# Optimization experiments

Measured on AMD Instinct MI355X. Metric: run time of the kernel, lower is better.

## Reference

```python
import jax, jax.numpy as jnp
import numpy as np

B, T, C, J = 2048, 128, 3, 25   # batch, frames, coords, joints
E = 64                          # structure elements (n_elements)


def setup_inputs() -> dict:
    key = jax.random.key(0)
    k1, k2 = jax.random.split(key)
    x = jax.random.normal(k1, (B, T, C, J), dtype=jnp.float32)
    centres = jax.random.uniform(k2, (E, 2), dtype=jnp.float32)
    sharpness = jnp.full((E, 2), 3.0, dtype=jnp.float32)  # torch init: ones*3
    return {"x": x, "centres": centres, "sharpness": sharpness}


def _mst_deaths(Dm):
    """Prim's MST over dense distance matrix Dm [n,n].
    The multiset of MST edge weights equals the finite death times of the
    0-dim Vietoris-Rips persistence diagram (births are all 0)."""
    n = Dm.shape[0]
    in_tree0 = jnp.zeros(n, dtype=bool).at[0].set(True)

    def step(carry, _):
        mind, in_tree = carry
        masked = jnp.where(in_tree, jnp.inf, mind)  # distance from tree to each node
        j = jnp.argmin(masked)
        w = masked[j]                               # weight of edge added to MST
        in_tree = in_tree.at[j].set(True)
        mind = jnp.minimum(mind, Dm[j])
        return (mind, in_tree), w

    (_, _), deaths = jax.lax.scan(step, (Dm[0], in_tree0), None, length=n - 1)
    return deaths  # [n-1]


def reference(x, centres, sharpness):
    # --- dense preprocessing ---
    h = x.mean(1)                           # [B, C, J]
    h = h[..., :, None] - h[..., None, :]   # [B, C, J, J] pairwise coord diffs
    h = h.mean(-3)                          # [B, J, J]
    h = jnp.sqrt((h * h).sum(axis=1))       # torch.norm(., 2, dim=1) -> [B, J]
    lo, hi = h.min(), h.max()
    rng = hi - lo
    safe = rng > 1e-8
    h = jnp.where(safe, (h - lo) / jnp.where(safe, rng, 1.0), jnp.zeros_like(h))

    # --- Vietoris-Rips dim-0 persistence on point cloud h: B points in J dims ---
    sq = (h * h).sum(-1)
    d2 = sq[:, None] + sq[None, :] - 2.0 * (h @ h.T)       # [B, B]
    Dm = jnp.sqrt(jnp.maximum(d2, 1e-12))
    deaths = _mst_deaths(Dm)                               # [B-1]
    pd = jnp.stack([jnp.zeros_like(deaths), deaths], -1)[None]  # [1, P, 2]

    # --- StructureElementLayer: out[b,e] = sum_p exp(-sum_d s[e,d]^2 (pd-c)^2) ---
    s2 = sharpness * sharpness                             # [E, 2]
    diff = pd[:, :, None, :] - centres[None, None, :, :]   # [1, P, E, 2]
    out = jnp.exp(-(diff * diff * s2).sum(-1)).sum(1)      # [1, E]
    return out
```

## Files before the change

### kernel.cpp

```cpp
#include <hip/hip_runtime.h>
#include <math.h>

#define B_N 2048
#define T_N 128
#define C_N 3
#define J_N 25
#define E_N 64
#define TC  (T_N*C_N)
#define TCJ (TC*J_N)
#define NQ4 (TCJ/4)
#define NC  128

#define D_OFF      0
#define H_OFF      (B_N*B_N)
#define BLO_OFF    (H_OFF + B_N*J_N)
#define BHI_OFF    (BLO_OFF + B_N)
#define DEATHS_OFF (BHI_OFF + B_N)
#define BEST_OFF   (DEATHS_OFF + B_N)
#define COMP_OFF   (BEST_OFF + 4*B_N)
#define GC_OFF     (COMP_OFF + 2*B_N)
#define DC_OFF     (GC_OFF + 2)

typedef unsigned long long u64;
#define U64MAX 0xFFFFFFFFFFFFFFFFull
#define U32INF 0xFFFFFFFFu

__global__ void __launch_bounds__(256) k_reduce(const float* __restrict__ x,
                                                float* __restrict__ ws) {
    __shared__ float4 part[250];
    __shared__ float S[100];
    __shared__ float Mj[25];
    const int t = threadIdx.x, b = blockIdx.x;
    const float4* x4 = (const float4*)(x + (size_t)b * TCJ);
    if (t < 250) {
        float4 a; a.x = a.y = a.z = a.w = 0.f;
        for (int idx = t; idx < NQ4; idx += 250) {
            float4 v = x4[idx];
            a.x += v.x; a.y += v.y; a.z += v.z; a.w += v.w;
        }
        part[t] = a;
    }
    __syncthreads();
    if (t < 25) {
        float4 s = part[t];
        #pragma unroll
        for (int g = 1; g < 10; ++g) {
            float4 v = part[t + 25 * g];
            s.x += v.x; s.y += v.y; s.z += v.z; s.w += v.w;
        }
        S[4*t] = s.x; S[4*t+1] = s.y; S[4*t+2] = s.z; S[4*t+3] = s.w;
    }
    __syncthreads();
    if (t < 25) Mj[t] = (S[t] + S[t+25] + S[t+50] + S[t+75]) * (1.0f / 384.0f);
    __syncthreads();
    if (t < 25) {
        float mj = Mj[t], acc = 0.f;
        #pragma unroll
        for (int i = 0; i < J_N; ++i) { float d = Mj[i] - mj; acc += d * d; }
        float hv = sqrtf(acc);
        ws[H_OFF + b * J_N + t] = hv;
        S[t] = hv;
    }
    __syncthreads();
    if (t == 0) {
        float lo = S[0], hi = S[0];
        #pragma unroll
        for (int i = 1; i < J_N; ++i) { lo = fminf(lo, S[i]); hi = fmaxf(hi, S[i]); }
        ws[BLO_OFF + b] = lo;
        ws[BHI_OFF + b] = hi;
    }
}

__global__ void __launch_bounds__(256) k_dist(float* ws) {
    __shared__ float A[32][27], Bsh[32][27];
    const int t = threadIdx.x;
    const int rowA = blockIdx.x * 32, rowB = blockIdx.y * 32;
    const float* h = ws + H_OFF;
    for (int idx = t; idx < 32 * J_N; idx += 256) {
        int r = idx / J_N, c = idx % J_N;
        A[r][c]   = h[(rowA + r) * J_N + c];
        Bsh[r][c] = h[(rowB + r) * J_N + c];
    }
    __syncthreads();
    const int tx = t & 31, ty = t >> 5;
    float* D = ws + D_OFF;
    #pragma unroll
    for (int rr = 0; rr < 4; ++rr) {
        const int r = ty + rr * 8;
        float acc = 0.f;
        #pragma unroll
        for (int k = 0; k < J_N; ++k) {
            float d = A[r][k] - Bsh[tx][k];
            acc += d * d;
        }
        D[(size_t)(rowA + r) * B_N + rowB + tx] = sqrtf(fmaxf(acc, 1e-12f));
    }
}

__global__ void __launch_bounds__(1024) k_scan0(float* __restrict__ ws) {
    const int t = threadIdx.x, w = t >> 6, lane = t & 63;
    const int row = blockIdx.x * 16 + w;
    const float4* row4 = (const float4*)(ws + D_OFF + (size_t)row * B_N);
    u64 best = U64MAX;
    #pragma unroll
    for (int k = 0; k < 8; ++k) {
        const int q = k * 64 + lane;
        float4 w4 = row4[q];
        const unsigned j0 = (unsigned)(q * 4);
        float wv[4] = {w4.x, w4.y, w4.z, w4.w};
        #pragma unroll
        for (int m = 0; m < 4; ++m) {
            unsigned j = j0 + m;
            if (j != (unsigned)row) {
                unsigned a = min((unsigned)row, j), b2 = max((unsigned)row, j);
                u64 key = ((u64)__float_as_uint(wv[m]) << 32) | (a << 11) | b2;
                if (key < best) best = key;
            }
        }
    }
    #pragma unroll
    for (int off = 32; off; off >>= 1) {
        u64 o = __shfl_down(best, off);
        if (o < best) best = o;
    }
    if (lane == 0) ((u64*)(ws + BEST_OFF))[row] = best;
    if (blockIdx.x < 16) ((unsigned*)(ws + DC_OFF))[blockIdx.x * 1024 + t] = U32INF;
    if (blockIdx.x == 0) {
        unsigned* gc = (unsigned*)(ws + COMP_OFF);
        gc[t] = (unsigned)t; gc[t + 1024] = (unsigned)(t + 1024);
        if (t == 0) { ((unsigned*)(ws + GC_OFF))[0] = 0u; ((unsigned*)(ws + GC_OFF))[1] = 0u; }
    }
}

__global__ void __launch_bounds__(1024) k_round(float* __restrict__ ws, int par_in) {
    unsigned* gcnt = (unsigned*)(ws + GC_OFF);
    const unsigned base = gcnt[par_in];
    if (base >= B_N - 1) return;
    __shared__ __align__(16) unsigned comp[B_N];
    __shared__ u64 cb[B_N];
    __shared__ unsigned par[B_N];
    __shared__ unsigned cnt_s;
    const int t = threadIdx.x, blk = blockIdx.x;
    const unsigned* gcomp_in = (const unsigned*)(ws + COMP_OFF) + par_in * B_N;
    unsigned* gcomp_out = (unsigned*)(ws + COMP_OFF) + (par_in ^ 1) * B_N;
    const u64* bin = (const u64*)(ws + BEST_OFF) + par_in * B_N;
    u64* bout = (u64*)(ws + BEST_OFF) + (par_in ^ 1) * B_N;
    float* deaths = ws + DEATHS_OFF;

    if (t == 0) cnt_s = 0u;
    comp[t] = gcomp_in[t]; comp[t + 1024] = gcomp_in[t + 1024];
    cb[t] = U64MAX; cb[t + 1024] = U64MAX;
    __syncthreads();
    #pragma unroll
    for (int i = t; i < B_N; i += 1024) {
        u64 bk = bin[i];
        if (bk != U64MAX) atomicMin(&cb[comp[i]], bk);
    }
    __syncthreads();
    #pragma unroll
    for (int c = t; c < B_N; c += 1024) {
        u64 k = cb[c];
        unsigned p = (unsigned)c;
        if (k != U64MAX) {
            unsigned a  = (unsigned)((k >> 11) & 0x7FFu);
            unsigned b2 = (unsigned)(k & 0x7FFu);
            unsigned ca = comp[a], cbv = comp[b2];
            unsigned c2 = (ca == (unsigned)c) ? cbv : ca;
            p = c2;
            if (!(cb[c2] == k && c2 < (unsigned)c)) {
                unsigned li = atomicAdd(&cnt_s, 1u);
                if (blk == 0) deaths[base + li] = __uint_as_float((unsigned)(k >> 32));
            }
        }
        par[c] = p;
    }
    __syncthreads();
    #pragma unroll
    for (int c = t; c < B_N; c += 1024) {
        unsigned p = par[c];
        if (p != (unsigned)c && par[p] == (unsigned)c && (unsigned)c < p) par[c] = (unsigned)c;
    }
    __syncthreads();
    #pragma unroll
    for (int c = t; c < B_N; c += 1024) {
        unsigned r = par[c];
        while (true) { unsigned pr = par[r]; if (pr == r) break; r = pr; }
        par[c] = r;
    }
    __syncthreads();
    #pragma unroll
    for (int i = t; i < B_N; i += 1024) comp[i] = par[comp[i]];
    __syncthreads();
    const unsigned newbase = base + cnt_s;
    if (blk == 0) {
        gcomp_out[t] = comp[t]; gcomp_out[t + 1024] = comp[t + 1024];
        if (t == 0) { gcnt[par_in ^ 1] = newbase; if (newbase >= B_N - 1) gcnt[par_in] = newbase; }
    }
    if (newbase >= B_N - 1) return;

    const int w = t >> 6, lane = t & 63;
    const int row = blk * 16 + w;
    const unsigned ci = comp[row];
    u64 prev = bin[row];
    {
        unsigned pa = (unsigned)((prev >> 11) & 0x7FFu);
        unsigned pb = (unsigned)(prev & 0x7FFu);
        unsigned jo = (pa == (unsigned)row) ? pb : pa;
        if (comp[jo] != ci) {
            if (lane == 0) bout[row] = prev;
            return;
        }
    }
    const float4* row4 = (const float4*)(ws + D_OFF + (size_t)row * B_N);
    const uint4* comp4 = (const uint4*)comp;
    u64 best = U64MAX;
    #pragma unroll
    for (int k = 0; k < 8; ++k) {
        const int q = k * 64 + lane;
        float4 w4 = row4[q];
        uint4  c4 = comp4[q];
        const unsigned j0 = (unsigned)(q * 4);
        float wv[4] = {w4.x, w4.y, w4.z, w4.w};
        unsigned cv[4] = {c4.x, c4.y, c4.z, c4.w};
        #pragma unroll
        for (int m = 0; m < 4; ++m) {
            if (cv[m] != ci) {
                unsigned j = j0 + m;
                unsigned a = min((unsigned)row, j), b2 = max((unsigned)row, j);
                u64 key = ((u64)__float_as_uint(wv[m]) << 32) | (a << 11) | b2;
                if (key < best) best = key;
            }
        }
    }
    #pragma unroll
    for (int off = 32; off; off >>= 1) {
        u64 o = __shfl_down(best, off);
        if (o < best) best = o;
    }
    if (lane == 0) bout[row] = best;
}

__global__ void __launch_bounds__(1024) k_round4c(float* __restrict__ ws) {
    unsigned* gcnt = (unsigned*)(ws + GC_OFF);
    const unsigned base = gcnt[1];
    if (base >= B_N - 1) return;
    __shared__ __align__(16) unsigned comp[B_N];
    __shared__ __align__(16) unsigned ovl[NC*NC];
    __shared__ unsigned cflag[B_N];
    __shared__ unsigned cnt_s, csum[16];
    u64* cb = (u64*)ovl;
    unsigned* par = ovl + 4096;
    const int t = threadIdx.x, blk = blockIdx.x;
    const unsigned* gcomp_in = (const unsigned*)(ws + COMP_OFF) + B_N;
    const u64* bin = (const u64*)(ws + BEST_OFF) + B_N;
    float* deaths = ws + DEATHS_OFF;

    if (t == 0) cnt_s = 0u;
    comp[t] = gcomp_in[t]; comp[t + 1024] = gcomp_in[t + 1024];
    cb[t] = U64MAX; cb[t + 1024] = U64MAX;
    __syncthreads();
    #pragma unroll
    for (int i = t; i < B_N; i += 1024) {
        u64 bk = bin[i];
        if (bk != U64MAX) atomicMin(&cb[comp[i]], bk);
    }
    __syncthreads();
    #pragma unroll
    for (int c = t; c < B_N; c += 1024) {
        u64 k = cb[c];
        unsigned p = (unsigned)c;
        if (k != U64MAX) {
            unsigned a  = (unsigned)((k >> 11) & 0x7FFu);
            unsigned b2 = (unsigned)(k & 0x7FFu);
            unsigned ca = comp[a], cbv = comp[b2];
            unsigned c2 = (ca == (unsigned)c) ? cbv : ca;
            p = c2;
            if (!(cb[c2] == k && c2 < (unsigned)c)) {
                unsigned li = atomicAdd(&cnt_s, 1u);
                if (blk == 0) deaths[base + li] = __uint_as_float((unsigned)(k >> 32));
            }
        }
        par[c] = p;
    }
    __syncthreads();
    #pragma unroll
    for (int c = t; c < B_N; c += 1024) {
        unsigned p = par[c];
        if (p != (unsigned)c && par[p] == (unsigned)c && (unsigned)c < p) par[c] = (unsigned)c;
    }
    __syncthreads();
    #pragma unroll
    for (int c = t; c < B_N; c += 1024) {
        unsigned r = par[c];
        while (true) { unsigned pr = par[r]; if (pr == r) break; r = pr; }
        par[c] = r;
    }
    __syncthreads();
    #pragma unroll
    for (int i = t; i < B_N; i += 1024) comp[i] = par[comp[i]];
    __syncthreads();
    const unsigned newbase = base + cnt_s;
    if (blk == 0 && t == 0) { gcnt[0] = newbase; gcnt[1] = newbase; }
    if (newbase >= B_N - 1) return;

    cflag[t] = 0u; cflag[t + 1024] = 0u;
    __syncthreads();
    cflag[comp[t]] = 1u; cflag[comp[t + 1024]] = 1u;
    __syncthreads();
    const unsigned lane = t & 63, w = t >> 6;
    unsigned f0 = cflag[2 * t], f1 = cflag[2 * t + 1];
    unsigned s = f0 + f1, sc = s;
    #pragma unroll
    for (int off = 1; off < 64; off <<= 1) {
        unsigned v = __shfl_up(sc, off);
        if (lane >= (unsigned)off) sc += v;
    }
    if (lane == 63) csum[w] = sc;
    __syncthreads();
    if (t < 16) {
        unsigned v = csum[t], acc = v;
        #pragma unroll
        for (int off = 1; off < 16; off <<= 1) {
            unsigned u2 = __shfl_up(acc, off);
            if (t >= off) acc += u2;
        }
        csum[t] = acc - v;
    }
    __syncthreads();
    unsigned off0 = csum[w] + (sc - s);
    __syncthreads();
    if (f0) cflag[2 * t] = off0;
    if (f1) cflag[2 * t + 1] = off0 + f0;
    __syncthreads();

    #pragma unroll
    for (int i = 0; i < 16; ++i) ovl[i * 1024 + t] = U32INF;
    __syncthreads();
    {
        const int row = blk * 16 + (int)w;
        const unsigned ci = comp[row];
        const unsigned ri = cflag[ci];
        const float4* row4 = (const float4*)(ws + D_OFF + (size_t)row * B_N);
        const uint4* comp4 = (const uint4*)comp;
        #pragma unroll
        for (int k = 0; k < 8; ++k) {
            const int q = k * 64 + (int)lane;
            float4 w4 = row4[q];
            uint4  c4 = comp4[q];
            float wv[4] = {w4.x, w4.y, w4.z, w4.w};
            unsigned cv[4] = {c4.x, c4.y, c4.z, c4.w};
            #pragma unroll
            for (int m = 0; m < 4; ++m) {
                if (cv[m] != ci) atomicMin(&ovl[ri * NC + cflag[cv[m]]], __float_as_uint(wv[m]));
            }
        }
    }
    __syncthreads();
    unsigned* gDc = (unsigned*)(ws + DC_OFF);
    #pragma unroll
    for (int i = t; i < NC * NC; i += 1024) {
        unsigned v = ovl[i];
        if (v != U32INF) atomicMin(&gDc[i], v);
    }
}

__global__ void __launch_bounds__(1024) k_finishstruct(float* __restrict__ ws,
                                                       const float* __restrict__ centres,
                                                       const float* __restrict__ sharp,
                                                       float* __restrict__ out) {
    __shared__ unsigned Dcs[NC * NC];
    __shared__ u64 cbf[NC];
    __shared__ unsigned parf[NC], ccomp[NC];
    __shared__ unsigned cnt_s, base_s;
    __shared__ float redlo[16], redhi[16];
    const int t = threadIdx.x;
    const int lane = t & 63, w = t >> 6;
    float* deaths = ws + DEATHS_OFF;
    const unsigned base0 = ((const unsigned*)(ws + GC_OFF))[0];

    if (base0 < B_N - 1) {
        const unsigned* gDc = (const unsigned*)(ws + DC_OFF);
        #pragma unroll
        for (int i = 0; i < 16; ++i) Dcs[i * 1024 + t] = gDc[i * 1024 + t];
        if (t < NC) ccomp[t] = (unsigned)t;
        if (t == 0) base_s = base0;
        __syncthreads();
        for (int iter = 0; iter < 7; ++iter) {
            if (t < NC) cbf[t] = U64MAX;
            if (t == 0) cnt_s = 0u;
            __syncthreads();
            #pragma unroll
            for (int q = 0; q < 8; ++q) {
                const int r = w * 8 + q;
                const unsigned cc = ccomp[r];
                u64 key = U64MAX;
                #pragma unroll
                for (int hh = 0; hh < 2; ++hh) {
                    const int c = lane + hh * 64;
                    unsigned wv = Dcs[r * NC + c];
                    if (wv != U32INF && ccomp[c] != cc) {
                        unsigned a = min((unsigned)r, (unsigned)c);
                        unsigned b2 = max((unsigned)r, (unsigned)c);
                        u64 k2 = ((u64)wv << 32) | (a << 7) | b2;
                        if (k2 < key) key = k2;
                    }
                }
                #pragma unroll
                for (int off = 32; off; off >>= 1) {
                    u64 o = __shfl_down(key, off);
                    if (o < key) key = o;
                }
                if (lane == 0 && key != U64MAX) atomicMin(&cbf[cc], key);
            }
            __syncthreads();
            bool add = false; float dw = 0.f;
            if (t < NC) {
                u64 k = cbf[t];
                unsigned p = (unsigned)t;
                if (k != U64MAX) {
                    unsigned a = (unsigned)((k >> 7) & 127u), b2 = (unsigned)(k & 127u);
                    unsigned ca = ccomp[a], cbv = ccomp[b2];
                    unsigned c2 = (ca == (unsigned)t) ? cbv : ca;
                    p = c2;
                    if (!(cbf[c2] == k && c2 < (unsigned)t)) {
                        add = true; dw = __uint_as_float((unsigned)(k >> 32));
                    }
                }
                parf[t] = p;
            }
            __syncthreads();
            if (t < NC) {
                unsigned pp = parf[t];
                if (pp != (unsigned)t && parf[pp] == (unsigned)t && (unsigned)t < pp) parf[t] = (unsigned)t;
            }
            __syncthreads();
            if (t < NC) {
                unsigned r2 = parf[t];
                while (parf[r2] != r2) r2 = parf[r2];
                parf[t] = r2;
            }
            __syncthreads();
            if (t < NC) {
                if (add) { unsigned li = atomicAdd(&cnt_s, 1u); deaths[base_s + li] = dw; }
                ccomp[t] = parf[ccomp[t]];
            }
            __syncthreads();
            if (t == 0) base_s += cnt_s;
            __syncthreads();
            if (base_s >= B_N - 1) break;
        }
        __threadfence_block();
        __syncthreads();
    }

    float lo = INFINITY, hi = -INFINITY;
    #pragma unroll
    for (int i = t; i < B_N; i += 1024) {
        lo = fminf(lo, ws[BLO_OFF + i]);
        hi = fmaxf(hi, ws[BHI_OFF + i]);
    }
    #pragma unroll
    for (int off = 32; off; off >>= 1) {
        lo = fminf(lo, __shfl_down(lo, off));
        hi = fmaxf(hi, __shfl_down(hi, off));
    }
    if (lane == 0) { redlo[w] = lo; redhi[w] = hi; }
    __syncthreads();
    lo = redlo[0]; hi = redhi[0];
    #pragma unroll
    for (int k = 1; k < 16; ++k) { lo = fminf(lo, redlo[k]); hi = fmaxf(hi, redhi[k]); }
    float rng = hi - lo;
    float rinv = (rng > 1e-8f) ? 1.0f / rng : 0.0f;

    for (int e = w; e < E_N; e += 16) {
        const float c0 = centres[e * 2], c1 = centres[e * 2 + 1];
        const float s0 = sharp[e * 2],   s1 = sharp[e * 2 + 1];
        const float s1sq = s1 * s1;
        float acc = 0.f;
        for (int p = lane; p < B_N - 1; p += 64) {
            float d = deaths[p] * rinv - c1;
            acc += expf(-s1sq * d * d);
        }
        #pragma unroll
        for (int off = 32; off; off >>= 1) acc += __shfl_down(acc, off);
        if (lane == 0) out[e] = expf(-s0 * s0 * c0 * c0) * acc;
    }
}

extern "C" void kernel_launch(void* const* d_in, const int* in_sizes, int n_in,
                              void* d_out, int out_size, void* d_ws, size_t ws_size,
                              hipStream_t stream) {
    const float* x       = (const float*)d_in[0];
    const float* centres = (const float*)d_in[1];
    const float* sharp   = (const float*)d_in[2];
    float* out = (float*)d_out;
    float* ws  = (float*)d_ws;

    hipLaunchKernelGGL(k_reduce,   dim3(B_N),    dim3(256),  0, stream, x, ws);
    hipLaunchKernelGGL(k_dist,     dim3(64, 64), dim3(256),  0, stream, ws);
    hipLaunchKernelGGL(k_scan0,    dim3(128),    dim3(1024), 0, stream, ws);
    hipLaunchKernelGGL(k_round,    dim3(128),    dim3(1024), 0, stream, ws, 0);
    hipLaunchKernelGGL(k_round,    dim3(128),    dim3(1024), 0, stream, ws, 1);
    hipLaunchKernelGGL(k_round,    dim3(128),    dim3(1024), 0, stream, ws, 0);
    hipLaunchKernelGGL(k_round4c,  dim3(128),    dim3(1024), 0, stream, ws);
    hipLaunchKernelGGL(k_finishstruct, dim3(1),  dim3(1024), 0, stream, ws, centres, sharp, out);
}
```

Measured before the change: 186.8 us.

## Fuse pairwise distance computation with first Boruvka min-edge scan

Merges the distance-matrix kernel and the initial per-row minimum-edge scan into one kernel, so each row's best edge key is computed while distances are produced. This removes a separate launch and a full re-read of the dense distance matrix. In exchange it uses a much smaller grid of large blocks with a big shared-memory tile of points, which lowers parallelism and may underfill the GPU.

```diff
diff --git a/kernel.cpp b/kernel.cpp
--- a/kernel.cpp
+++ b/kernel.cpp
@@ -71,65 +71,57 @@
     }
 }
 
-__global__ void __launch_bounds__(256) k_dist(float* ws) {
-    __shared__ float A[32][27], Bsh[32][27];
-    const int t = threadIdx.x;
-    const int rowA = blockIdx.x * 32, rowB = blockIdx.y * 32;
+__global__ void __launch_bounds__(1024) k_distscan(float* __restrict__ ws) {
+    __shared__ float A[16][26];
+    __shared__ float Bsh[1024 * J_N];
+    const int t = threadIdx.x, blk = blockIdx.x;
+    const int ty = t >> 6, tx = t & 63;
     const float* h = ws + H_OFF;
-    for (int idx = t; idx < 32 * J_N; idx += 256) {
-        int r = idx / J_N, c = idx % J_N;
-        A[r][c]   = h[(rowA + r) * J_N + c];
-        Bsh[r][c] = h[(rowB + r) * J_N + c];
-    }
-    __syncthreads();
-    const int tx = t & 31, ty = t >> 5;
-    float* D = ws + D_OFF;
-    #pragma unroll
-    for (int rr = 0; rr < 4; ++rr) {
-        const int r = ty + rr * 8;
-        float acc = 0.f;
-        #pragma unroll
-        for (int k = 0; k < J_N; ++k) {
-            float d = A[r][k] - Bsh[tx][k];
-            acc += d * d;
-        }
-        D[(size_t)(rowA + r) * B_N + rowB + tx] = sqrtf(fmaxf(acc, 1e-12f));
-    }
-}
-
-__global__ void __launch_bounds__(1024) k_scan0(float* __restrict__ ws) {
-    const int t = threadIdx.x, w = t >> 6, lane = t & 63;
-    const int row = blockIdx.x * 16 + w;
-    const float4* row4 = (const float4*)(ws + D_OFF + (size_t)row * B_N);
-    u64 best = U64MAX;
-    #pragma unroll
-    for (int k = 0; k < 8; ++k) {
-        const int q = k * 64 + lane;
-        float4 w4 = row4[q];
-        const unsigned j0 = (unsigned)(q * 4);
-        float wv[4] = {w4.x, w4.y, w4.z, w4.w};
-        #pragma unroll
-        for (int m = 0; m < 4; ++m) {
-            unsigned j = j0 + m;
-            if (j != (unsigned)row) {
-                unsigned a = min((unsigned)row, j), b2 = max((unsigned)row, j);
-                u64 key = ((u64)__float_as_uint(wv[m]) << 32) | (a << 11) | b2;
-                if (key < best) best = key;
-            }
-        }
-    }
-    #pragma unroll
-    for (int off = 32; off; off >>= 1) {
-        u64 o = __shfl_down(best, off);
-        if (o < best) best = o;
-    }
-    if (lane == 0) ((u64*)(ws + BEST_OFF))[row] = best;
-    if (blockIdx.x < 16) ((unsigned*)(ws + DC_OFF))[blockIdx.x * 1024 + t] = U32INF;
-    if (blockIdx.x == 0) {
+    const int row0 = blk * 16;
+    for (int idx = t; idx < 16 * J_N; idx += 1024)
+        A[idx / J_N][idx % J_N] = h[(row0 + idx / J_N) * J_N + idx % J_N];
+    if (blk < 16) ((unsigned*)(ws + DC_OFF))[blk * 1024 + t] = U32INF;
+    if (blk == 0) {
         unsigned* gc = (unsigned*)(ws + COMP_OFF);
         gc[t] = (unsigned)t; gc[t + 1024] = (unsigned)(t + 1024);
         if (t == 0) { ((unsigned*)(ws + GC_OFF))[0] = 0u; ((unsigned*)(ws + GC_OFF))[1] = 0u; }
     }
+    const int row = row0 + ty;
+    float ar[J_N];
+    u64 bestk = U64MAX;
+    float* D = ws + D_OFF;
+    for (int mt = 0; mt < 2; ++mt) {
+        __syncthreads();
+        for (int idx = t; idx < 1024 * J_N; idx += 1024)
+            Bsh[idx] = h[mt * 1024 * J_N + idx];
+        __syncthreads();
+        if (mt == 0) {
+            #pragma unroll
+            for (int k = 0; k < J_N; ++k) ar[k] = A[ty][k];
+        }
+        #pragma unroll 4
+        for (int cc = 0; cc < 16; ++cc) {
+            const int col = mt * 1024 + cc * 64 + tx;
+            const float* bp = &Bsh[(cc * 64 + tx) * J_N];
+            float acc = 0.f;
+            #pragma unroll
+            for (int k = 0; k < J_N; ++k) { float d = ar[k] - bp[k]; acc += d * d; }
+            float dist = sqrtf(fmaxf(acc, 1e-12f));
+            D[(size_t)row * B_N + col] = dist;
+            if (col != row) {
+                unsigned a = min((unsigned)row, (unsigned)col);
+                unsigned b2 = max((unsigned)row, (unsigned)col);
+                u64 key = ((u64)__float_as_uint(dist) << 32) | (a << 11) | b2;
+                if (key < bestk) bestk = key;
+            }
+        }
+    }
+    #pragma unroll
+    for (int off = 32; off; off >>= 1) {
+        u64 o = __shfl_down(bestk, off);
+        if (o < bestk) bestk = o;
+    }
+    if (tx == 0) ((u64*)(ws + BEST_OFF))[row] = bestk;
 }
 
 __global__ void __launch_bounds__(1024) k_round(float* __restrict__ ws, int par_in) {
@@ -496,12 +488,11 @@
     float* out = (float*)d_out;
     float* ws  = (float*)d_ws;
 
-    hipLaunchKernelGGL(k_reduce,   dim3(B_N),    dim3(256),  0, stream, x, ws);
-    hipLaunchKernelGGL(k_dist,     dim3(64, 64), dim3(256),  0, stream, ws);
-    hipLaunchKernelGGL(k_scan0,    dim3(128),    dim3(1024), 0, stream, ws);
-    hipLaunchKernelGGL(k_round,    dim3(128),    dim3(1024), 0, stream, ws, 0);
-    hipLaunchKernelGGL(k_round,    dim3(128),    dim3(1024), 0, stream, ws, 1);
-    hipLaunchKernelGGL(k_round,    dim3(128),    dim3(1024), 0, stream, ws, 0);
-    hipLaunchKernelGGL(k_round4c,  dim3(128),    dim3(1024), 0, stream, ws);
-    hipLaunchKernelGGL(k_finishstruct, dim3(1),  dim3(1024), 0, stream, ws, centres, sharp, out);
-}
+    hipLaunchKernelGGL(k_reduce,   dim3(B_N),  dim3(256),  0, stream, x, ws);
+    hipLaunchKernelGGL(k_distscan, dim3(128),  dim3(1024), 0, stream, ws);
+    hipLaunchKernelGGL(k_round,    dim3(128),  dim3(1024), 0, stream, ws, 0);
+    hipLaunchKernelGGL(k_round,    dim3(128),  dim3(1024), 0, stream, ws, 1);
+    hipLaunchKernelGGL(k_round,    dim3(128),  dim3(1024), 0, stream, ws, 0);
+    hipLaunchKernelGGL(k_round4c,  dim3(128),  dim3(1024), 0, stream, ws);
+    hipLaunchKernelGGL(k_finishstruct, dim3(1), dim3(1024), 0, stream, ws, centres, sharp, out);
+}
```

New measurement: 183.4 us. About the same (-1.8%).
